# Optimization experiments

Hardware: AMD Instinct MI355X
Metric: run time of the kernel (lower is better)

The kernel has to match this reference:

```python
import jax, jax.numpy as jnp
import numpy as np

B, Q, C, H, N, D, F = 1, 2048, 2048, 1024, 16, 64, 4096
R = Q + C  # relative position encoding length
EPS = 1e-12
NEG = 1e30


def setup_inputs() -> dict:
    key = jax.random.key(0)
    ks = jax.random.split(key, 16)
    s = 0.02
    return dict(
        content_stream=jax.random.normal(ks[0], (B, Q, H), jnp.float32),
        content_mask=jnp.zeros((B, 1, Q, C), jnp.float32),
        context=jax.random.normal(ks[1], (B, C, H), jnp.float32),
        position_encoding=jax.random.normal(ks[2], (B, R, H), jnp.float32),
        content_bias=jax.random.normal(ks[3], (N, D), jnp.float32) * s,
        position_bias=jax.random.normal(ks[4], (N, D), jnp.float32) * s,
        segment_encoding=jax.random.normal(ks[5], (2, N, D), jnp.float32) * s,
        segment_matrix=jax.random.randint(ks[6], (B, Q, C), 0, 2).astype(bool),
        segment_bias=jax.random.normal(ks[7], (N, D), jnp.float32) * s,
        Wq=jax.random.normal(ks[8], (H, N, D), jnp.float32) * s,
        Wk=jax.random.normal(ks[9], (H, N, D), jnp.float32) * s,
        Wv=jax.random.normal(ks[10], (H, N, D), jnp.float32) * s,
        Wr=jax.random.normal(ks[11], (H, N, D), jnp.float32) * s,
        Wo=jax.random.normal(ks[12], (H, N, D), jnp.float32) * s,
        ln1_gamma=jnp.ones((H,), jnp.float32),
        ln1_beta=jnp.zeros((H,), jnp.float32),
        W1=jax.random.normal(ks[13], (H, F), jnp.float32) * s,
        b1=jnp.zeros((F,), jnp.float32),
        W2=jax.random.normal(ks[14], (F, H), jnp.float32) * s,
        b2=jnp.zeros((H,), jnp.float32),
        ln2_gamma=jnp.ones((H,), jnp.float32),
        ln2_beta=jnp.zeros((H,), jnp.float32),
    )


def _layernorm(x, g, b):
    m = jnp.mean(x, axis=-1, keepdims=True)
    v = jnp.mean(jnp.square(x - m), axis=-1, keepdims=True)
    return (x - m) * jax.lax.rsqrt(v + EPS) * g + b


def _rel_shift(x, klen):
    # x: [b, n, q, r] -> shifted [b, n, q, klen] (XLNet reshape trick)
    b, n, q, r = x.shape
    x = x.reshape(b, n, r, q)[:, :, 1:, :].reshape(b, n, q, r - 1)
    return x[:, :, :, :klen]


def reference(content_stream, content_mask, context, position_encoding,
              content_bias, position_bias, segment_encoding, segment_matrix,
              segment_bias, Wq, Wk, Wv, Wr, Wo, ln1_gamma, ln1_beta,
              W1, b1, W2, b2, ln2_gamma, ln2_beta):
    q = jnp.einsum('bqh,hnd->bqnd', content_stream, Wq)
    k = jnp.einsum('bch,hnd->bcnd', context, Wk)
    v = jnp.einsum('bch,hnd->bcnd', context, Wv)
    r = jnp.einsum('brh,hnd->brnd', position_encoding, Wr)

    # content / position / segment bias terms (XLNet relative attention)
    ac = jnp.einsum('bqnd,bcnd->bnqc', q + content_bias, k)
    bd = _rel_shift(jnp.einsum('bqnd,brnd->bnqr', q + position_bias, r),
                    k.shape[1])
    ef = jnp.einsum('bqnd,snd->bnqs', q + segment_bias, segment_encoding)
    ef = jnp.where(segment_matrix[:, None], ef[..., 1:], ef[..., :1])

    scores = (ac + bd + ef) / jnp.sqrt(jnp.float32(D))
    scores = scores - NEG * content_mask  # mask: 1.0 = disallowed
    probs = jax.nn.softmax(scores, axis=-1)

    attn = jnp.einsum('bnqc,bcnd->bqnd', probs, v)
    attn_out = jnp.einsum('bqnd,hnd->bqh', attn, Wo)

    # residual + LN, then FFN, residual + LN (dropout off: training=False)
    ffn_in = _layernorm(attn_out + content_stream, ln1_gamma, ln1_beta)
    ffn_out = jax.nn.relu(ffn_in @ W1 + b1) @ W2 + b2
    return _layernorm(ffn_out + ffn_in, ln2_gamma, ln2_beta)
```

## Files before the change

### kernel.cpp

```cpp
#include <hip/hip_runtime.h>
#include <stdint.h>


typedef unsigned short ushort_t;
typedef __attribute__((ext_vector_type(8))) short bf16x8;
typedef __attribute__((ext_vector_type(4))) float f32x4;

#define QLEN 2048
#define CLEN 2048
#define HDIM 1024
#define NHEAD 16
#define DHEAD 64
#define RLEN 4096
#define FDIM 4096

__device__ __forceinline__ float bf2f(ushort_t u) {
  union { float f; uint32_t i; } x; x.i = ((uint32_t)u) << 16; return x.f;
}
__device__ __forceinline__ ushort_t f2bf(float f) {
  union { float f; uint32_t i; } x; x.f = f;
  uint32_t r = x.i + 0x7fffu + ((x.i >> 16) & 1u);
  return (ushort_t)(r >> 16);
}
__device__ __forceinline__ float u2f(uint32_t u) {
  union { float f; uint32_t i; } x; x.i = u; return x.f;
}
__device__ __forceinline__ f32x4 mfma16(bf16x8 a, bf16x8 b, f32x4 c) {
  return __builtin_amdgcn_mfma_f32_16x16x32_bf16(a, b, c, 0, 0, 0);
}
__device__ __forceinline__ bool probe_bf16(const uint32_t* probe) {
  return probe[0] == 0x3F803F80u;
}

typedef const __attribute__((address_space(1))) void* gas_t;
typedef __attribute__((address_space(3))) void* las_t;
__device__ __forceinline__ void glds16(const void* g, void* l) {
  __builtin_amdgcn_global_load_lds((gas_t)(uintptr_t)g, (las_t)(uintptr_t)l, 16, 0, 0);
}

__device__ __forceinline__ void bar_lds() {
  __asm__ volatile("s_waitcnt lgkmcnt(0)\n\ts_barrier" ::: "memory");
}
__device__ __forceinline__ void bar_full() {
  __asm__ volatile("s_waitcnt vmcnt(0) lgkmcnt(0)\n\ts_barrier" ::: "memory");
}

struct ConvJobs {
  const void* src[5];
  const void* mask_src;
  ushort_t* dst[5];
  int n[5];
  int blk0[6];
};

__global__ __launch_bounds__(256) void conv_all(
    ConvJobs J, const uint32_t* __restrict__ probe)
{
  const bool isb = probe_bf16(probe);
  int j = 0;
  #pragma unroll
  for (int t = 1; t < 5; t++) if ((int)blockIdx.x >= J.blk0[t]) j = t;
  const int lb = blockIdx.x - J.blk0[j];
  const int nb = J.blk0[j + 1] - J.blk0[j];
  const int n = J.n[j];
  ushort_t* dst = J.dst[j];
  if (j < 4) {
    const void* src = J.src[j];
    for (int i = lb * 256 + threadIdx.x; i < n; i += nb * 256)
      dst[i] = isb ? ((const ushort_t*)src)[i] : f2bf(((const float*)src)[i]);
  } else {
    const void* sm = J.src[4];
    uint32_t sw = 0;
    #pragma unroll
    for (int t = 0; t < 8; t++) sw |= ((const uint32_t*)sm)[t];
    const bool i8 = sw > 1u;
    for (int i = lb * 256 + threadIdx.x; i < n; i += nb * 256) {
      const int s = i8 ? (int)((const unsigned char*)sm)[i]
                       : (int)((const uint32_t*)sm)[i];
      const float mv = isb ? bf2f(((const ushort_t*)J.mask_src)[i])
                           : ((const float*)J.mask_src)[i];
      const float f = (float)(s ? 1 : 0) + (mv != 0.f ? 2.f : 0.f);
      dst[i] = f2bf(f);
    }
  }
}

struct SmallBatch {
  const void* src[10];
  int n[10];
  int off[10];
};

__global__ __launch_bounds__(256) void convert_small(
    SmallBatch sb, ushort_t* __restrict__ dst, const uint32_t* __restrict__ probe)
{
  const bool isb = probe_bf16(probe);
  const int t = blockIdx.x;
  const void* s = sb.src[t];
  ushort_t* d = dst + sb.off[t];
  for (int i = threadIdx.x; i < sb.n[t]; i += 256)
    d[i] = isb ? ((const ushort_t*)s)[i] : f2bf(((const float*)s)[i]);
}

struct TransJobs { const void* src[4]; ushort_t* dst[4]; };
__global__ __launch_bounds__(256) void transpose4_to_bf16(
    TransJobs T, int R, int C, const uint32_t* __restrict__ probe)
{
  const bool isb = probe_bf16(probe);
  const void* in = T.src[blockIdx.z];
  ushort_t* out = T.dst[blockIdx.z];
  __shared__ ushort_t t[32][33];
  const int bx = blockIdx.x * 32, by = blockIdx.y * 32;
  const int x = threadIdx.x & 31, y0 = threadIdx.x >> 5;
  #pragma unroll
  for (int yy = 0; yy < 32; yy += 8) {
    const size_t idx = (size_t)(by + y0 + yy) * C + bx + x;
    t[y0 + yy][x] = isb ? ((const ushort_t*)in)[idx] : f2bf(((const float*)in)[idx]);
  }
  __syncthreads();
  #pragma unroll
  for (int yy = 0; yy < 32; yy += 8)
    out[(size_t)(bx + y0 + yy) * R + by + x] = t[x][y0 + yy];
}

__global__ __launch_bounds__(256) void transpose_to_bf16(
    const void* __restrict__ in, ushort_t* __restrict__ out, int R, int C,
    const uint32_t* __restrict__ probe)
{
  const bool isb = probe_bf16(probe);
  __shared__ ushort_t t[32][33];
  const int bx = blockIdx.x * 32, by = blockIdx.y * 32;
  const int x = threadIdx.x & 31, y0 = threadIdx.x >> 5;
  #pragma unroll
  for (int yy = 0; yy < 32; yy += 8) {
    const size_t idx = (size_t)(by + y0 + yy) * C + bx + x;
    t[y0 + yy][x] = isb ? ((const ushort_t*)in)[idx] : f2bf(((const float*)in)[idx]);
  }
  __syncthreads();
  #pragma unroll
  for (int yy = 0; yy < 32; yy += 8)
    out[(size_t)(bx + y0 + yy) * R + by + x] = t[x][y0 + yy];
}

__device__ __forceinline__ void gemm_store(
    void* out, const ushort_t* bias, int M, int N, int epi,
    int gm, int gn, float v)
{
  if (epi == 0) {
    ((ushort_t*)out)[(size_t)gm * N + gn] = f2bf(v);
  } else if (epi == 1) {
    ((ushort_t*)out)[(size_t)gn * M + gm] = f2bf(v);
  } else if (epi == 2) {
    ((float*)out)[(size_t)gm * N + gn] = v;
  } else if (epi == 3) {
    v += bf2f(bias[gn]); v = v > 0.f ? v : 0.f;
    ((ushort_t*)out)[(size_t)gm * N + gn] = f2bf(v);
  } else if (epi == 4) {
    v += bf2f(bias[gn]);
    ((float*)out)[(size_t)gm * N + gn] = v;
  } else if (epi == 5) {
    ((ushort_t*)out)[((size_t)(gn >> 6) * M + gm) * 64 + (gn & 63)] = f2bf(v);
  } else {
    if (gn < 1024)
      ((ushort_t*)out)[((size_t)(gn >> 6) * M + gm) * 64 + (gn & 63)] = f2bf(v);
    else
      ((ushort_t*)out)[(size_t)2097152 + (size_t)(gn - 1024) * M + gm] = f2bf(v);
  }
}

struct Ptr4 { void* p[4]; };
__global__ __launch_bounds__(256) void gemm128_bt_kernel(
    const ushort_t* __restrict__ A, const ushort_t* __restrict__ Bt,
    const ushort_t* __restrict__ bias, Ptr4 outs,
    int M, int N, int K, int Kc, int epi)
{
  __shared__ __attribute__((aligned(16))) ushort_t As[2][128 * 32];
  __shared__ __attribute__((aligned(16))) ushort_t Bs[2][128 * 32];
  const int tid = threadIdx.x;
  const int lane = tid & 63, wave = tid >> 6;
  const int l15 = lane & 15, quad = lane >> 4;
  const int wm = wave >> 1, wn = wave & 1;
  const int m0 = blockIdx.y * 128, n0 = blockIdx.x * 128;
  const int kb = blockIdx.z * Kc;
  void* out = outs.p[blockIdx.z];

  const int arow = tid >> 2;
  const int acol = (tid & 3) * 8;

  f32x4 acc[4][4];
  #pragma unroll
  for (int i = 0; i < 4; i++)
    #pragma unroll
    for (int j = 0; j < 4; j++) acc[i][j] = (f32x4){0.f, 0.f, 0.f, 0.f};

  const int KI = Kc >> 5;
  glds16(&A[(size_t)(m0 + arow) * K + kb + acol], &As[0][tid * 8]);
  glds16(&A[(size_t)(m0 + arow + 64) * K + kb + acol], &As[0][tid * 8 + 2048]);
  glds16(&Bt[(size_t)(n0 + arow) * K + kb + acol], &Bs[0][tid * 8]);
  glds16(&Bt[(size_t)(n0 + arow + 64) * K + kb + acol], &Bs[0][tid * 8 + 2048]);
  bar_full();

  for (int ki = 0; ki < KI; ki++) {
    const int b = ki & 1;
    if (ki + 1 < KI) {
      const int k1 = kb + ((ki + 1) << 5);
      glds16(&A[(size_t)(m0 + arow) * K + k1 + acol], &As[b ^ 1][tid * 8]);
      glds16(&A[(size_t)(m0 + arow + 64) * K + k1 + acol], &As[b ^ 1][tid * 8 + 2048]);
      glds16(&Bt[(size_t)(n0 + arow) * K + k1 + acol], &Bs[b ^ 1][tid * 8]);
      glds16(&Bt[(size_t)(n0 + arow + 64) * K + k1 + acol], &Bs[b ^ 1][tid * 8 + 2048]);
    }
    bf16x8 af[4], bfr[4];
    #pragma unroll
    for (int i = 0; i < 4; i++)
      af[i] = *(const bf16x8*)&As[b][(wm * 64 + i * 16 + l15) * 32 + quad * 8];
    #pragma unroll
    for (int j = 0; j < 4; j++)
      bfr[j] = *(const bf16x8*)&Bs[b][(wn * 64 + j * 16 + l15) * 32 + quad * 8];
    #pragma unroll
    for (int i = 0; i < 4; i++)
      #pragma unroll
      for (int j = 0; j < 4; j++)
        acc[i][j] = mfma16(af[i], bfr[j], acc[i][j]);
    bar_full();
  }

  #pragma unroll
  for (int i = 0; i < 4; i++)
    #pragma unroll
    for (int j = 0; j < 4; j++)
      #pragma unroll
      for (int rg = 0; rg < 4; rg++)
        gemm_store(out, bias, M, N, epi,
                   m0 + wm * 64 + i * 16 + quad * 4 + rg,
                   n0 + wn * 64 + j * 16 + l15, acc[i][j][rg]);
}

struct MultiG {
  const ushort_t* A[3]; const ushort_t* Bt[3]; void* out[3];
  int M[3], N[3], epi[3], bxsh[3], blk0[4];
};

__global__ __launch_bounds__(256) void gemm128_multi_kernel(MultiG G, int K)
{
  int j = 0;
  #pragma unroll
  for (int t = 1; t < 3; t++) if ((int)blockIdx.x >= G.blk0[t]) j = t;
  const int lb = blockIdx.x - G.blk0[j];
  const int bx = lb & ((1 << G.bxsh[j]) - 1);
  const int by = lb >> G.bxsh[j];
  const ushort_t* __restrict__ A = G.A[j];
  const ushort_t* __restrict__ Bt = G.Bt[j];
  void* out = G.out[j];
  const int M = G.M[j], N = G.N[j], epi = G.epi[j];

  __shared__ __attribute__((aligned(16))) ushort_t As[2][128 * 32];
  __shared__ __attribute__((aligned(16))) ushort_t Bs[2][128 * 32];
  const int tid = threadIdx.x;
  const int lane = tid & 63, wave = tid >> 6;
  const int l15 = lane & 15, quad = lane >> 4;
  const int wm = wave >> 1, wn = wave & 1;
  const int m0 = by * 128, n0 = bx * 128;

  const int arow = tid >> 2;
  const int acol = (tid & 3) * 8;

  f32x4 acc[4][4];
  #pragma unroll
  for (int i = 0; i < 4; i++)
    #pragma unroll
    for (int jj = 0; jj < 4; jj++) acc[i][jj] = (f32x4){0.f, 0.f, 0.f, 0.f};

  const int KI = K >> 5;
  glds16(&A[(size_t)(m0 + arow) * K + acol], &As[0][tid * 8]);
  glds16(&A[(size_t)(m0 + arow + 64) * K + acol], &As[0][tid * 8 + 2048]);
  glds16(&Bt[(size_t)(n0 + arow) * K + acol], &Bs[0][tid * 8]);
  glds16(&Bt[(size_t)(n0 + arow + 64) * K + acol], &Bs[0][tid * 8 + 2048]);
  bar_full();

  for (int ki = 0; ki < KI; ki++) {
    const int b = ki & 1;
    if (ki + 1 < KI) {
      const int k1 = (ki + 1) << 5;
      glds16(&A[(size_t)(m0 + arow) * K + k1 + acol], &As[b ^ 1][tid * 8]);
      glds16(&A[(size_t)(m0 + arow + 64) * K + k1 + acol], &As[b ^ 1][tid * 8 + 2048]);
      glds16(&Bt[(size_t)(n0 + arow) * K + k1 + acol], &Bs[b ^ 1][tid * 8]);
      glds16(&Bt[(size_t)(n0 + arow + 64) * K + k1 + acol], &Bs[b ^ 1][tid * 8 + 2048]);
    }
    bf16x8 af[4], bfr[4];
    #pragma unroll
    for (int i = 0; i < 4; i++)
      af[i] = *(const bf16x8*)&As[b][(wm * 64 + i * 16 + l15) * 32 + quad * 8];
    #pragma unroll
    for (int jj = 0; jj < 4; jj++)
      bfr[jj] = *(const bf16x8*)&Bs[b][(wn * 64 + jj * 16 + l15) * 32 + quad * 8];
    #pragma unroll
    for (int i = 0; i < 4; i++)
      #pragma unroll
      for (int jj = 0; jj < 4; jj++)
        acc[i][jj] = mfma16(af[i], bfr[jj], acc[i][jj]);
    bar_full();
  }

  #pragma unroll
  for (int i = 0; i < 4; i++)
    #pragma unroll
    for (int jj = 0; jj < 4; jj++)
      #pragma unroll
      for (int rg = 0; rg < 4; rg++)
        gemm_store(out, nullptr, M, N, epi,
                   m0 + wm * 64 + i * 16 + quad * 4 + rg,
                   n0 + wn * 64 + jj * 16 + l15, acc[i][jj][rg]);
}

__global__ __launch_bounds__(256) void gemm64_bt_kernel(
    const ushort_t* __restrict__ A, const ushort_t* __restrict__ Bt,
    const ushort_t* __restrict__ bias, void* __restrict__ out,
    int M, int N, int K, int epi)
{
  __shared__ __attribute__((aligned(16))) ushort_t As[2][64 * 32];
  __shared__ __attribute__((aligned(16))) ushort_t Bs[2][64 * 32];
  const int tid = threadIdx.x;
  const int lane = tid & 63, wave = tid >> 6;
  const int l15 = lane & 15, quad = lane >> 4;
  const int wm = wave >> 1, wn = wave & 1;
  const int m0 = blockIdx.y * 64, n0 = blockIdx.x * 64;

  const int arow = tid >> 2;
  const int acol = (tid & 3) * 8;

  f32x4 acc[2][2];
  #pragma unroll
  for (int i = 0; i < 2; i++)
    #pragma unroll
    for (int j = 0; j < 2; j++) acc[i][j] = (f32x4){0.f, 0.f, 0.f, 0.f};

  const int KI = K >> 5;
  glds16(&A[(size_t)(m0 + arow) * K + acol], &As[0][tid * 8]);
  glds16(&Bt[(size_t)(n0 + arow) * K + acol], &Bs[0][tid * 8]);
  bar_full();

  for (int ki = 0; ki < KI; ki++) {
    const int b = ki & 1;
    if (ki + 1 < KI) {
      const int k1 = (ki + 1) << 5;
      glds16(&A[(size_t)(m0 + arow) * K + k1 + acol], &As[b ^ 1][tid * 8]);
      glds16(&Bt[(size_t)(n0 + arow) * K + k1 + acol], &Bs[b ^ 1][tid * 8]);
    }
    bf16x8 af[2], bfr[2];
    #pragma unroll
    for (int i = 0; i < 2; i++)
      af[i] = *(const bf16x8*)&As[b][(wm * 32 + i * 16 + l15) * 32 + quad * 8];
    #pragma unroll
    for (int j = 0; j < 2; j++)
      bfr[j] = *(const bf16x8*)&Bs[b][(wn * 32 + j * 16 + l15) * 32 + quad * 8];
    #pragma unroll
    for (int i = 0; i < 2; i++)
      #pragma unroll
      for (int j = 0; j < 2; j++)
        acc[i][j] = mfma16(af[i], bfr[j], acc[i][j]);
    bar_full();
  }

  #pragma unroll
  for (int i = 0; i < 2; i++)
    #pragma unroll
    for (int j = 0; j < 2; j++)
      #pragma unroll
      for (int rg = 0; rg < 4; rg++)
        gemm_store(out, bias, M, N, epi,
                   m0 + wm * 32 + i * 16 + quad * 4 + rg,
                   n0 + wn * 32 + j * 16 + l15, acc[i][j][rg]);
}

#define ESTR 36
#define PSTR2 72
__global__ __launch_bounds__(512, 4) void attn_flash(
    const ushort_t* __restrict__ qh, const ushort_t* __restrict__ kh,
    const ushort_t* __restrict__ vT, const ushort_t* __restrict__ rh,
    const ushort_t* __restrict__ cbias, const ushort_t* __restrict__ pbias,
    const ushort_t* __restrict__ sbias, const ushort_t* __restrict__ senc,
    const ushort_t* __restrict__ fmb, ushort_t* __restrict__ attn)
{
  __shared__ __attribute__((aligned(16))) ushort_t kbuf[2][64 * 64];
  __shared__ __attribute__((aligned(16))) ushort_t vbuf[2][64 * 64];
  __shared__ __attribute__((aligned(16))) ushort_t rbuf[2][96 * 64];
  __shared__ __attribute__((aligned(16))) ushort_t Pbuf[32 * PSTR2];
  __shared__ __attribute__((aligned(16))) float escr[8 * 16 * ESTR];
  __shared__ float wsum[2][4][16];
  __shared__ float e0s[32], e1s[32];

  const int n = blockIdx.x;
  const int q0 = blockIdx.y * 32;
  const int tid = threadIdx.x;
  const int lane = tid & 63, wave = tid >> 6;
  const int l15 = lane & 15, quad = lane >> 4;
  const int hq = wave >> 2, ct = wave & 3;

  const ushort_t* qn = qh + (size_t)n * QLEN * 64;
  const ushort_t* kn = kh + (size_t)n * CLEN * 64;
  const ushort_t* rn = rh + (size_t)n * RLEN * 64;
  const ushort_t* vn = vT + (size_t)n * 64 * CLEN;

  const int srow = lane >> 3;
  const int sg = (lane & 7) ^ srow;

  ushort_t* qpcS = (ushort_t*)escr;
  ushort_t* qppS = qpcS + 32 * 64;
  for (int idx = tid; idx < 32 * 64; idx += 512) {
    const int row = idx >> 6, col = idx & 63;
    const float qv = bf2f(qn[(size_t)(q0 + row) * 64 + col]);
    qpcS[idx] = f2bf(qv + bf2f(cbias[n * DHEAD + col]));
    qppS[idx] = f2bf(qv + bf2f(pbias[n * DHEAD + col]));
  }
  if (wave == 7) {
    const int row = lane & 31, sidx = lane >> 5;
    float a = 0.f;
    for (int d = 0; d < DHEAD; d++)
      a += (bf2f(qn[(size_t)(q0 + row) * 64 + d]) + bf2f(sbias[n * DHEAD + d]))
           * bf2f(senc[(size_t)(sidx * NHEAD + n) * DHEAD + d]);
    if (sidx == 0) e0s[row] = a; else e1s[row] = a;
  }
  __syncthreads();

  const bf16x8* qpc8 = (const bf16x8*)qpcS;
  const bf16x8* qpp8 = (const bf16x8*)qppS;
  const bf16x8 qcf0 = qpc8[(hq * 16 + l15) * 8 + quad];
  const bf16x8 qcf1 = qpc8[(hq * 16 + l15) * 8 + 4 + quad];
  const bf16x8 qpf0 = qpp8[(hq * 16 + l15) * 8 + quad];
  const bf16x8 qpf1 = qpp8[(hq * 16 + l15) * 8 + 4 + quad];

  const ushort_t* gsrc;
  size_t sstride, sadv;
  bool s4;
  ushort_t *d0, *d1;
  if (wave < 2) {
    const int r0 = wave * 32;
    gsrc = kn + (size_t)(r0 + srow) * 64 + sg * 8;
    sstride = 512; sadv = 4096; s4 = true;
    d0 = &kbuf[0][r0 * 64]; d1 = &kbuf[1][r0 * 64];
  } else if (wave < 4) {
    const int r0 = (wave - 2) * 32;
    gsrc = vn + (size_t)(r0 + srow) * CLEN + sg * 8;
    sstride = (size_t)8 * CLEN; sadv = 64; s4 = true;
    d0 = &vbuf[0][r0 * 64]; d1 = &vbuf[1][r0 * 64];
  } else {
    const int r0 = (wave - 4) * 24;
    gsrc = rn + (size_t)(QLEN - 32 - q0 + r0 + srow) * 64 + sg * 8;
    sstride = 512; sadv = 4096; s4 = false;
    d0 = &rbuf[0][r0 * 64]; d1 = &rbuf[1][r0 * 64];
  }

  #define STAGE(D) do { \
    glds16(gsrc, (D)); \
    glds16(gsrc + sstride, (D) + 512); \
    glds16(gsrc + 2 * sstride, (D) + 1024); \
    if (s4) glds16(gsrc + 3 * sstride, (D) + 1536); \
    gsrc += sadv; } while (0)

  STAGE(d0);
  bar_full();

  const float e0v = e0s[hq * 16 + l15], e1v = e1s[hq * 16 + l15];
  const float a0q = e0v * 0.125f;
  const float adq = (e1v - e0v) * 0.125f;

  float* escr_w = escr + wave * (16 * ESTR);
  const int gk0 = quad ^ (l15 & 7);
  const int gk1 = (quad + 4) ^ (l15 & 7);

  float l_row = 0.f;
  f32x4 O = (f32x4){0.f, 0.f, 0.f, 0.f};

  const ushort_t* fmp = fmb + (size_t)(q0 + hq * 16 + l15) * CLEN + ct * 16 + quad * 4;

  #define DO_CHUNK(kb, rb, vb, FMV) do { \
    _Pragma("unroll") \
    for (int t = 0; t < 2; t++) { \
      const int rrow = ct * 16 + ((1 - hq) + t) * 16 + l15; \
      f32x4 e = (f32x4){0.f, 0.f, 0.f, 0.f}; \
      e = mfma16(*(const bf16x8*)&(rb)[rrow * 64 + gk0 * 8], qpf0, e); \
      e = mfma16(*(const bf16x8*)&(rb)[rrow * 64 + gk1 * 8], qpf1, e); \
      *(f32x4*)&escr_w[l15 * ESTR + t * 16 + quad * 4] = e; \
    } \
    const int krow = ct * 16 + l15; \
    f32x4 a = (f32x4){0.f, 0.f, 0.f, 0.f}; \
    a = mfma16(*(const bf16x8*)&(kb)[krow * 64 + gk0 * 8], qcf0, a); \
    a = mfma16(*(const bf16x8*)&(kb)[krow * 64 + gk1 * 8], qcf1, a); \
    float fv4[4]; \
    fv4[0] = u2f(FMV.x << 16); fv4[1] = u2f(FMV.x & 0xFFFF0000u); \
    fv4[2] = u2f(FMV.y << 16); fv4[3] = u2f(FMV.y & 0xFFFF0000u); \
    const float* dg = &escr_w[l15 * ESTR + quad * 4 - l15 + 16]; \
    float p[4], psum = 0.f; \
    _Pragma("unroll") \
    for (int rg = 0; rg < 4; rg++) { \
      const float f = fv4[rg]; \
      const float mk = floorf(f * 0.5f); \
      const float sm = f - 2.f * mk; \
      float v = fmaf(a[rg] + dg[rg], 0.125f, fmaf(sm, adq, a0q)); \
      v = fmaf(mk, -1.0e30f, v); \
      p[rg] = __expf(v); \
      psum += p[rg]; \
    } \
    psum += __shfl_xor(psum, 16); \
    psum += __shfl_xor(psum, 32); \
    l_row += psum; \
    { uint32_t pk0, pk1; \
      asm("v_cvt_pk_bf16_f32 %0, %1, %2" : "=v"(pk0) : "v"(p[0]), "v"(p[1])); \
      asm("v_cvt_pk_bf16_f32 %0, %1, %2" : "=v"(pk1) : "v"(p[2]), "v"(p[3])); \
      uint2 pkk; pkk.x = pk0; pkk.y = pk1; \
      *(uint2*)&Pbuf[(hq * 16 + l15) * PSTR2 + ct * 16 + quad * 4] = pkk; } \
    bar_lds(); \
    { const int vrow = ct * 16 + l15; \
      const bf16x8 vf0 = *(const bf16x8*)&(vb)[vrow * 64 + gk0 * 8]; \
      const bf16x8 vf1 = *(const bf16x8*)&(vb)[vrow * 64 + gk1 * 8]; \
      const bf16x8 pa0 = *(const bf16x8*)&Pbuf[(hq * 16 + l15) * PSTR2 + quad * 8]; \
      const bf16x8 pa1 = *(const bf16x8*)&Pbuf[(hq * 16 + l15) * PSTR2 + 32 + quad * 8]; \
      O = mfma16(pa0, vf0, O); \
      O = mfma16(pa1, vf1, O); } \
    bar_full(); \
  } while (0)

  for (int ci = 0; ci < CLEN / 64; ci += 2) {
    const uint2 fmva = *(const uint2*)fmp;
    const uint2 fmvb = *(const uint2*)(fmp + 64);
    fmp += 128;
    STAGE(d1);
    DO_CHUNK(kbuf[0], rbuf[0], vbuf[0], fmva);
    if (ci + 2 < CLEN / 64) STAGE(d0);
    DO_CHUNK(kbuf[1], rbuf[1], vbuf[1], fmvb);
  }
  #undef DO_CHUNK
  #undef STAGE

  if (quad == 0) wsum[hq][ct][l15] = l_row;
  __syncthreads();
  const float l = wsum[hq][0][l15] + wsum[hq][1][l15] + wsum[hq][2][l15] + wsum[hq][3][l15];
  const float linv = 1.0f / l;
  float linv4[4];
  #pragma unroll
  for (int rg = 0; rg < 4; rg++) linv4[rg] = __shfl(linv, quad * 4 + rg);
  #pragma unroll
  for (int rg = 0; rg < 4; rg++)
    attn[(size_t)(q0 + hq * 16 + quad * 4 + rg) * HDIM + n * 64 + ct * 16 + l15] =
        f2bf(O[rg] * linv4[rg]);
}

__global__ __launch_bounds__(256) void ln_kernel(
    const float* __restrict__ x0, const float* __restrict__ x1,
    const float* __restrict__ x2, const float* __restrict__ x3,
    const ushort_t* __restrict__ res_bf, const float* __restrict__ res_f,
    const ushort_t* __restrict__ badd,
    const ushort_t* __restrict__ gamma, const ushort_t* __restrict__ beta,
    ushort_t* __restrict__ out_bf, float* __restrict__ out_f,
    void* __restrict__ out_dyn, const uint32_t* __restrict__ probe)
{
  const int row = blockIdx.x, tid = threadIdx.x;
  const int lane = tid & 63, wave = tid >> 6;
  __shared__ float red[8];
  const size_t base = (size_t)row * HDIM;
  float v[4];
  #pragma unroll
  for (int i = 0; i < 4; i++) {
    const int h = tid + i * 256;
    float xv = x0[base + h];
    if (x1) xv += x1[base + h] + x2[base + h] + x3[base + h];
    if (badd) xv += bf2f(badd[h]);
    const float rv = res_bf ? bf2f(res_bf[base + h]) : res_f[base + h];
    v[i] = xv + rv;
  }
  float s = v[0] + v[1] + v[2] + v[3];
  float ss = v[0] * v[0] + v[1] * v[1] + v[2] * v[2] + v[3] * v[3];
  #pragma unroll
  for (int off = 32; off > 0; off >>= 1) {
    s += __shfl_xor(s, off);
    ss += __shfl_xor(ss, off);
  }
  if (lane == 0) { red[wave] = s; red[4 + wave] = ss; }
  __syncthreads();
  s = red[0] + red[1] + red[2] + red[3];
  ss = red[4] + red[5] + red[6] + red[7];
  const float mean = s * (1.0f / HDIM);
  float var = ss * (1.0f / HDIM) - mean * mean;
  var = var > 0.f ? var : 0.f;
  const float rs = rsqrtf(var + 1e-12f);
  const bool outb = out_dyn ? probe_bf16(probe) : false;
  #pragma unroll
  for (int i = 0; i < 4; i++) {
    const int h = tid + i * 256;
    const float y = (v[i] - mean) * rs * bf2f(gamma[h]) + bf2f(beta[h]);
    if (out_bf) out_bf[base + h] = f2bf(y);
    if (out_f)  out_f[base + h] = y;
    if (out_dyn) {
      if (outb) ((ushort_t*)out_dyn)[base + h] = f2bf(y);
      else      ((float*)out_dyn)[base + h] = y;
    }
  }
}

extern "C" void kernel_launch(void* const* d_in, const int* in_sizes, int n_in,
                              void* d_out, int out_size, void* d_ws, size_t ws_size,
                              hipStream_t stream)
{
  (void)in_sizes; (void)n_in; (void)out_size; (void)ws_size;

  const void* cs_r   = d_in[0];
  const void* mask_r = d_in[1];
  const void* ctx_r  = d_in[2];
  const void* pe_r   = d_in[3];
  const void* cb_r   = d_in[4];
  const void* pb_r   = d_in[5];
  const void* senc_r = d_in[6];
  const void* smat   = d_in[7];
  const void* sb_r   = d_in[8];
  const void* Wq_r   = d_in[9];
  const void* Wk_r   = d_in[10];
  const void* Wv_r   = d_in[11];
  const void* Wr_r   = d_in[12];
  const void* Wo_r   = d_in[13];
  const void* g1_r   = d_in[14];
  const void* be1_r  = d_in[15];
  const void* W1_r   = d_in[16];
  const void* b1_r   = d_in[17];
  const void* W2_r   = d_in[18];
  const void* b2_r   = d_in[19];
  const void* g2_r   = d_in[20];
  const void* be2_r  = d_in[21];

  const uint32_t* probe = (const uint32_t*)g1_r;

  char* w = (char*)d_ws;
  #define WSOFF(mb) ((void*)(w + ((size_t)(mb) << 20)))
  ushort_t* fm_b     = (ushort_t*)WSOFF(0);
  ushort_t* Wqt      = (ushort_t*)WSOFF(8);
  ushort_t* Wkt      = (ushort_t*)WSOFF(10);
  ushort_t* Wvt      = (ushort_t*)WSOFF(12);
  ushort_t* Wrt      = (ushort_t*)WSOFF(14);
  ushort_t* W1t      = (ushort_t*)WSOFF(16);
  ushort_t* W2t      = (ushort_t*)WSOFF(24);
  ushort_t* Wo_b     = (ushort_t*)WSOFF(32);
  ushort_t* smalls   = (ushort_t*)WSOFF(34);
  ushort_t* cs_b     = (ushort_t*)WSOFF(35);
  ushort_t* ctx_b    = (ushort_t*)WSOFF(47);
  ushort_t* pe_b     = (ushort_t*)WSOFF(51);
  ushort_t* qbuf     = (ushort_t*)WSOFF(59);
  ushort_t* kbuf     = (ushort_t*)WSOFF(63);
  ushort_t* vTbuf    = (ushort_t*)WSOFF(67);
  ushort_t* rbuf     = (ushort_t*)WSOFF(71);
  ushort_t* attnbuf  = (ushort_t*)WSOFF(79);
  float*    attn_out = (float*)WSOFF(83);
  ushort_t* ffn_in_b = (ushort_t*)WSOFF(91);
  ushort_t* hidden   = (ushort_t*)WSOFF(39);
  float*    ffn_in_f = (float*)WSOFF(71);
  float*    fp0      = (float*)WSOFF(0);
  float*    fp1      = (float*)WSOFF(8);
  float*    fp2      = (float*)WSOFF(59);
  float*    fp3      = (float*)WSOFF(83);

  ushort_t* cb   = smalls + 0;
  ushort_t* pb   = smalls + 1024;
  ushort_t* sb   = smalls + 2048;
  ushort_t* senc = smalls + 3072;
  ushort_t* b1   = smalls + 5120;
  ushort_t* b2   = smalls + 9216;
  ushort_t* g1   = smalls + 10240;
  ushort_t* be1  = smalls + 11264;
  ushort_t* g2   = smalls + 12288;
  ushort_t* be2  = smalls + 13312;

  const dim3 blk(256);

  SmallBatch sbatch;
  const void* ssrc[10] = {cb_r, pb_r, sb_r, senc_r, b1_r, b2_r, g1_r, be1_r, g2_r, be2_r};
  const int   sn[10]   = {1024, 1024, 1024, 2048, 4096, 1024, 1024, 1024, 1024, 1024};
  const int   soff[10] = {0, 1024, 2048, 3072, 5120, 9216, 10240, 11264, 12288, 13312};
  for (int i = 0; i < 10; i++) { sbatch.src[i] = ssrc[i]; sbatch.n[i] = sn[i]; sbatch.off[i] = soff[i]; }
  convert_small<<<10, blk, 0, stream>>>(sbatch, smalls, probe);

  ConvJobs cj;
  cj.src[0] = cs_r;  cj.dst[0] = cs_b;  cj.n[0] = QLEN * HDIM;
  cj.src[1] = ctx_r; cj.dst[1] = ctx_b; cj.n[1] = CLEN * HDIM;
  cj.src[2] = pe_r;  cj.dst[2] = pe_b;  cj.n[2] = RLEN * HDIM;
  cj.src[3] = Wo_r;  cj.dst[3] = Wo_b;  cj.n[3] = HDIM * HDIM;
  cj.src[4] = smat;  cj.dst[4] = fm_b;  cj.n[4] = QLEN * CLEN;
  cj.mask_src = mask_r;
  int pfx = 0;
  for (int i = 0; i < 5; i++) {
    cj.blk0[i] = pfx;
    pfx += (cj.n[i] + 2047) / 2048;
  }
  cj.blk0[5] = pfx;
  conv_all<<<pfx, blk, 0, stream>>>(cj, probe);

  TransJobs tj;
  tj.src[0] = Wq_r; tj.dst[0] = Wqt;
  tj.src[1] = Wk_r; tj.dst[1] = Wkt;
  tj.src[2] = Wv_r; tj.dst[2] = Wvt;
  tj.src[3] = Wr_r; tj.dst[3] = Wrt;
  transpose4_to_bf16<<<dim3(32, 32, 4), blk, 0, stream>>>(tj, HDIM, HDIM, probe);
  transpose_to_bf16<<<dim3(128, 32), blk, 0, stream>>>(W1_r, W1t, HDIM, FDIM, probe);
  transpose_to_bf16<<<dim3(32, 128), blk, 0, stream>>>(W2_r, W2t, FDIM, HDIM, probe);

  MultiG mg;
  mg.A[0] = cs_b;  mg.Bt[0] = Wqt; mg.out[0] = qbuf; mg.M[0] = QLEN; mg.N[0] = HDIM; mg.epi[0] = 5; mg.bxsh[0] = 3;
  mg.A[1] = ctx_b; mg.Bt[1] = Wkt; mg.out[1] = kbuf; mg.M[1] = CLEN; mg.N[1] = 2048; mg.epi[1] = 6; mg.bxsh[1] = 4;
  mg.A[2] = pe_b;  mg.Bt[2] = Wrt; mg.out[2] = rbuf; mg.M[2] = RLEN; mg.N[2] = HDIM; mg.epi[2] = 5; mg.bxsh[2] = 3;
  mg.blk0[0] = 0; mg.blk0[1] = 128; mg.blk0[2] = 384; mg.blk0[3] = 640;
  gemm128_multi_kernel<<<dim3(640), blk, 0, stream>>>(mg, HDIM);

  attn_flash<<<dim3(NHEAD, QLEN / 32), dim3(512), 0, stream>>>(
      qbuf, kbuf, vTbuf, rbuf, cb, pb, sb, senc, fm_b, attnbuf);

  gemm64_bt_kernel<<<dim3(16, 32), blk, 0, stream>>>(attnbuf, Wo_b, nullptr, attn_out, QLEN, HDIM, HDIM, 2);

  ln_kernel<<<QLEN, blk, 0, stream>>>(attn_out, nullptr, nullptr, nullptr,
                                      cs_b, nullptr, nullptr, g1, be1,
                                      ffn_in_b, ffn_in_f, nullptr, probe);

  Ptr4 o1; o1.p[0] = hidden; o1.p[1] = o1.p[2] = o1.p[3] = nullptr;
  gemm128_bt_kernel<<<dim3(32, 16, 1), blk, 0, stream>>>(
      ffn_in_b, W1t, b1, o1, QLEN, FDIM, HDIM, HDIM, 3);

  Ptr4 o2; o2.p[0] = fp0; o2.p[1] = fp1; o2.p[2] = fp2; o2.p[3] = fp3;
  gemm128_bt_kernel<<<dim3(8, 16, 4), blk, 0, stream>>>(
      hidden, W2t, nullptr, o2, QLEN, HDIM, FDIM, FDIM / 4, 2);

  ln_kernel<<<QLEN, blk, 0, stream>>>(fp0, fp1, fp2, fp3,
                                      nullptr, ffn_in_f, b2, g2, be2,
                                      nullptr, nullptr, d_out, probe);
  #undef WSOFF
}
```

Measured before the change: 459.7 us.

## Feed P from registers into PV MFMA, drop LDS P buffer and mid-chunk barrier

```diff
diff --git a/kernel.cpp b/kernel.cpp
--- a/kernel.cpp
+++ b/kernel.cpp
@@ -373,7 +373,6 @@
 }
 
 #define ESTR 36
-#define PSTR2 72
 __global__ __launch_bounds__(512, 4) void attn_flash(
     const ushort_t* __restrict__ qh, const ushort_t* __restrict__ kh,
     const ushort_t* __restrict__ vT, const ushort_t* __restrict__ rh,
@@ -384,7 +383,6 @@
   __shared__ __attribute__((aligned(16))) ushort_t kbuf[2][64 * 64];
   __shared__ __attribute__((aligned(16))) ushort_t vbuf[2][64 * 64];
   __shared__ __attribute__((aligned(16))) ushort_t rbuf[2][96 * 64];
-  __shared__ __attribute__((aligned(16))) ushort_t Pbuf[32 * PSTR2];
   __shared__ __attribute__((aligned(16))) float escr[8 * 16 * ESTR];
   __shared__ float wsum[2][4][16];
   __shared__ float e0s[32], e1s[32];
@@ -467,9 +465,13 @@
   float* escr_w = escr + wave * (16 * ESTR);
   const int gk0 = quad ^ (l15 & 7);
   const int gk1 = (quad + 4) ^ (l15 & 7);
+  const int vcol = ((ct * 2 + (quad >> 1)) ^ (l15 & 7)) * 8 + (quad & 1) * 4;
 
   float l_row = 0.f;
-  f32x4 O = (f32x4){0.f, 0.f, 0.f, 0.f};
+  f32x4 O0 = (f32x4){0.f, 0.f, 0.f, 0.f};
+  f32x4 O1 = (f32x4){0.f, 0.f, 0.f, 0.f};
+  f32x4 O2 = (f32x4){0.f, 0.f, 0.f, 0.f};
+  f32x4 O3 = (f32x4){0.f, 0.f, 0.f, 0.f};
 
   const ushort_t* fmp = fmb + (size_t)(q0 + hq * 16 + l15) * CLEN + ct * 16 + quad * 4;
 
@@ -490,7 +492,7 @@
     fv4[0] = u2f(FMV.x << 16); fv4[1] = u2f(FMV.x & 0xFFFF0000u); \
     fv4[2] = u2f(FMV.y << 16); fv4[3] = u2f(FMV.y & 0xFFFF0000u); \
     const float* dg = &escr_w[l15 * ESTR + quad * 4 - l15 + 16]; \
-    float p[4], psum = 0.f; \
+    float p[4]; \
     _Pragma("unroll") \
     for (int rg = 0; rg < 4; rg++) { \
       const float f = fv4[rg]; \
@@ -499,24 +501,23 @@
       float v = fmaf(a[rg] + dg[rg], 0.125f, fmaf(sm, adq, a0q)); \
       v = fmaf(mk, -1.0e30f, v); \
       p[rg] = __expf(v); \
-      psum += p[rg]; \
+      l_row += p[rg]; \
     } \
-    psum += __shfl_xor(psum, 16); \
-    psum += __shfl_xor(psum, 32); \
-    l_row += psum; \
-    { uint32_t pk0, pk1; \
-      asm("v_cvt_pk_bf16_f32 %0, %1, %2" : "=v"(pk0) : "v"(p[0]), "v"(p[1])); \
-      asm("v_cvt_pk_bf16_f32 %0, %1, %2" : "=v"(pk1) : "v"(p[2]), "v"(p[3])); \
-      uint2 pkk; pkk.x = pk0; pkk.y = pk1; \
-      *(uint2*)&Pbuf[(hq * 16 + l15) * PSTR2 + ct * 16 + quad * 4] = pkk; } \
-    bar_lds(); \
-    { const int vrow = ct * 16 + l15; \
-      const bf16x8 vf0 = *(const bf16x8*)&(vb)[vrow * 64 + gk0 * 8]; \
-      const bf16x8 vf1 = *(const bf16x8*)&(vb)[vrow * 64 + gk1 * 8]; \
-      const bf16x8 pa0 = *(const bf16x8*)&Pbuf[(hq * 16 + l15) * PSTR2 + quad * 8]; \
-      const bf16x8 pa1 = *(const bf16x8*)&Pbuf[(hq * 16 + l15) * PSTR2 + 32 + quad * 8]; \
-      O = mfma16(pa0, vf0, O); \
-      O = mfma16(pa1, vf1, O); } \
+    uint32_t pk0, pk1; \
+    asm("v_cvt_pk_bf16_f32 %0, %1, %2" : "=v"(pk0) : "v"(p[0]), "v"(p[1])); \
+    asm("v_cvt_pk_bf16_f32 %0, %1, %2" : "=v"(pk1) : "v"(p[2]), "v"(p[3])); \
+    union { bf16x8 v; uint32_t u[4]; } au; \
+    au.u[0] = pk0; au.u[1] = pk1; au.u[2] = 0u; au.u[3] = 0u; \
+    _Pragma("unroll") \
+    for (int dt = 0; dt < 4; dt++) { \
+      const uint2 vv = *(const uint2*)&(vb)[(dt * 16 + l15) * 64 + vcol]; \
+      union { bf16x8 v; uint32_t u[4]; } bu; \
+      bu.u[0] = vv.x; bu.u[1] = vv.y; bu.u[2] = vv.x; bu.u[3] = vv.y; \
+      if (dt == 0) O0 = mfma16(au.v, bu.v, O0); \
+      else if (dt == 1) O1 = mfma16(au.v, bu.v, O1); \
+      else if (dt == 2) O2 = mfma16(au.v, bu.v, O2); \
+      else O3 = mfma16(au.v, bu.v, O3); \
+    } \
     bar_full(); \
   } while (0)
 
@@ -532,7 +533,18 @@
   #undef DO_CHUNK
   #undef STAGE
 
-  if (quad == 0) wsum[hq][ct][l15] = l_row;
+  float ps = l_row;
+  ps += __shfl_xor(ps, 16);
+  ps += __shfl_xor(ps, 32);
+  if (quad == 0) wsum[hq][ct][l15] = ps;
+  float* obuf = hq ? (float*)vbuf : (float*)kbuf;
+  #pragma unroll
+  for (int rg = 0; rg < 4; rg++) {
+    obuf[(ct * 16 + quad * 4 + rg) * 64 +  0 + l15] = O0[rg];
+    obuf[(ct * 16 + quad * 4 + rg) * 64 + 16 + l15] = O1[rg];
+    obuf[(ct * 16 + quad * 4 + rg) * 64 + 32 + l15] = O2[rg];
+    obuf[(ct * 16 + quad * 4 + rg) * 64 + 48 + l15] = O3[rg];
+  }
   __syncthreads();
   const float l = wsum[hq][0][l15] + wsum[hq][1][l15] + wsum[hq][2][l15] + wsum[hq][3][l15];
   const float linv = 1.0f / l;
@@ -540,9 +552,12 @@
   #pragma unroll
   for (int rg = 0; rg < 4; rg++) linv4[rg] = __shfl(linv, quad * 4 + rg);
   #pragma unroll
-  for (int rg = 0; rg < 4; rg++)
-    attn[(size_t)(q0 + hq * 16 + quad * 4 + rg) * HDIM + n * 64 + ct * 16 + l15] =
-        f2bf(O[rg] * linv4[rg]);
+  for (int rg = 0; rg < 4; rg++) {
+    const int qq = quad * 4 + rg, dd = ct * 16 + l15;
+    const float s = obuf[(0 * 16 + qq) * 64 + dd] + obuf[(1 * 16 + qq) * 64 + dd]
+                  + obuf[(2 * 16 + qq) * 64 + dd] + obuf[(3 * 16 + qq) * 64 + dd];
+    attn[(size_t)(q0 + hq * 16 + qq) * HDIM + n * 64 + dd] = f2bf(s * linv4[rg]);
+  }
 }
 
 __global__ __launch_bounds__(256) void ln_kernel(
```

Result: no change. 454.4 us (-1.1%).
